# Kernel tuning notes

Hardware: AMD Instinct MI355X
Metric: run time of the kernel (lower is better)

The kernel has to match this reference:

```python
import jax, jax.numpy as jnp
import numpy as np

# dims matching init_kwargs
L, D, NH = 4, 1024, 16          # num_blocks, embed_dim, num_heads
HD = D // NH                     # head dim
CUR, MEM, BS, IN = 512, 512, 8, 512
FF = 4 * D
GRU_BIAS = 2.0

def sinusoidal_pe(full_seq, dim):
    # SinusoidalPE: freqs = arange(0, dim, 2); inv = 10000**(-freqs/dim); seq descending
    freqs = jnp.arange(0, dim, 2.0)
    inv = 10000.0 ** (-freqs / dim)
    seq = jnp.arange(full_seq - 1, -1, -1.0)
    ang = seq[:, None] * inv[None, :]                       # (full, dim/2)
    return jnp.concatenate([jnp.sin(ang), jnp.cos(ang)], axis=-1)  # (full, dim)

def layer_norm(x, g, b, eps=1e-5):
    m = x.mean(-1, keepdims=True)
    v = ((x - m) ** 2).mean(-1, keepdims=True)
    return (x - m) * jax.lax.rsqrt(v + eps) * g + b

def rel_shift(x):
    # Transformer-XL relative shift. x: (q, k, b, h)
    q, k, b, h = x.shape
    zp = jnp.zeros((q, 1, b, h), x.dtype)
    return jnp.concatenate([zp, x], axis=1).reshape(k + 1, q, b, h)[1:].reshape(q, k, b, h)

def gru_gate(x, y, W):
    # W: (6, D, D) = Wr, Ur, Wz, Uz, Wg, Ug (no bias except learned-ish gru_bias on z)
    Wr, Ur, Wz, Uz, Wg, Ug = W[0], W[1], W[2], W[3], W[4], W[5]
    r = jax.nn.sigmoid(y @ Wr.T + x @ Ur.T)
    z = jax.nn.sigmoid(y @ Wz.T + x @ Uz.T - GRU_BIAS)
    hh = jnp.tanh(y @ Wg.T + (r * x) @ Ug.T)
    return (1.0 - z) * x + z * hh

def rel_attn(q, k, v, pos, U, V, mask, W):
    # q: (cur, bs, D); k, v: (full, bs, D); pos: (full, D); W: (5, D, D) = Wq,Wk,Wv,Wr,Wo
    cur, bs, _ = q.shape
    full = k.shape[0]
    qh = (q @ W[0].T).reshape(cur, bs, NH, HD)
    kh = (k @ W[1].T).reshape(full, bs, NH, HD)
    vh = (v @ W[2].T).reshape(full, bs, NH, HD)
    rh = (pos @ W[3].T).reshape(full, NH, HD)
    AC = jnp.einsum('ibhd,jbhd->ijbh', qh + U, kh)          # content stream with U bias
    BD = rel_shift(jnp.einsum('ibhd,jhd->ijbh', qh + V, rh))  # position stream with V bias
    score = (AC + BD) * (1.0 / np.sqrt(HD))
    score = jnp.where(mask[:, :, None, None], jnp.asarray(-1e30, score.dtype), score)
    attn = jax.nn.softmax(score, axis=1)
    out = jnp.einsum('ijbh,jbhd->ibhd', attn, vh).reshape(cur, bs, D)
    return out @ W[4].T

def gelu(x):
    return jax.nn.gelu(x, approximate=False)  # torch nn.GELU default is exact

def _forward(h, memory, W_emb, b_emb, U, V, ln1, ln2, Wattn, g1, g2, fc_W1, fc_b1, fc_W2, fc_b2):
    h = jnp.transpose(h, (1, 0, 2))            # (cur, bs, in)
    mem = jax.lax.stop_gradient(memory)        # memory holds detached hidden states
    cur = h.shape[0]
    prev = mem.shape[1]
    full = cur + prev
    x = gelu(h @ W_emb.T + b_emb)              # linear embedding + GELU activation
    pos = sinusoidal_pe(full, D)               # (full, D); pos_emb.unsqueeze(1) broadcast over bs
    mask = jnp.triu(jnp.ones((cur, full), bool), 1 + prev)
    out = x
    for i in range(L):
        key = jnp.concatenate([mem[i], out], axis=0)   # (full, bs, D)
        nq = layer_norm(out, ln1[i, 0], ln1[i, 1])
        nk = layer_norm(key, ln1[i, 0], ln1[i, 1])
        Y = rel_attn(nq, nk, nk, pos, U, V, mask, Wattn[i])
        Y = gelu(Y)                                     # dropout is identity (eval / p=0)
        o1 = gru_gate(out, Y, g1[i])
        E = layer_norm(o1, ln2[i, 0], ln2[i, 1])
        E = gelu(gelu(E @ fc_W1[i].T + fc_b1[i]) @ fc_W2[i].T + fc_b2[i])
        out = gru_gate(o1, E, g2[i])
    return jnp.transpose(out, (1, 0, 2))       # (bs, cur, D)

def setup_inputs() -> dict:
    key = jax.random.key(0)
    ks = jax.random.split(key, 12)
    s = 0.02
    eye2 = jnp.stack([jnp.ones(D, jnp.float32), jnp.zeros(D, jnp.float32)])  # (gamma, beta)
    return {
        'h': jax.random.normal(ks[0], (BS, CUR, IN), jnp.float32),
        'memory': jax.random.normal(ks[1], (L, MEM, BS, D), jnp.float32),
        'W_emb': jax.random.normal(ks[2], (D, IN), jnp.float32) * s,
        'b_emb': jnp.zeros((D,), jnp.float32),
        'U': jax.random.normal(ks[3], (NH, HD), jnp.float32) * s,
        'V': jax.random.normal(ks[4], (NH, HD), jnp.float32) * s,
        'ln1': jnp.tile(eye2[None], (L, 1, 1)),
        'ln2': jnp.tile(eye2[None], (L, 1, 1)),
        'Wattn': jax.random.normal(ks[5], (L, 5, D, D), jnp.float32) * s,  # q,k,v,r,o per block
        'g1': jax.random.normal(ks[6], (L, 6, D, D), jnp.float32) * s,
        'g2': jax.random.normal(ks[7], (L, 6, D, D), jnp.float32) * s,
        'fc_W1': jax.random.normal(ks[8], (L, FF, D), jnp.float32) * s,
        'fc_b1': jnp.zeros((L, FF), jnp.float32),
        'fc_W2': jax.random.normal(ks[9], (L, D, FF), jnp.float32) * s,
        'fc_b2': jnp.zeros((L, D), jnp.float32),
    }

def reference(h, memory, W_emb, b_emb, U, V, ln1, ln2, Wattn, g1, g2, fc_W1, fc_b1, fc_W2, fc_b2):
    return _forward(h, memory, W_emb, b_emb, U, V, ln1, ln2, Wattn, g1, g2, fc_W1, fc_b1, fc_W2, fc_b2)
```

## Files before the change

### kernel.cpp

```cpp
#include <hip/hip_runtime.h>
#include <hip/hip_bf16.h>


typedef __attribute__((ext_vector_type(8))) __bf16 bfrag;
typedef __attribute__((ext_vector_type(4))) float f4;
typedef __attribute__((ext_vector_type(4))) unsigned short u16x4;
typedef __attribute__((ext_vector_type(8))) unsigned short u16x8;

__device__ __forceinline__ unsigned short f2bf(float f){
  union { float f; unsigned u; } v; v.f = f;
  unsigned r = v.u + 0x7fffu + ((v.u >> 16) & 1u);
  return (unsigned short)(r >> 16);
}
__device__ __forceinline__ float bf2f(unsigned short u){
  union { unsigned u; float f; } v; v.u = (unsigned)u << 16; return v.f;
}
__device__ __forceinline__ float geluf(float x){
  return 0.5f * x * (1.0f + erff(x * 0.7071067811865476f));
}
__device__ __forceinline__ float sigm(float x){ return 1.0f/(1.0f + __expf(-x)); }

__device__ __forceinline__ void gl_lds(const void* g, void* l){
  __builtin_amdgcn_global_load_lds(
    reinterpret_cast<const __attribute__((address_space(1))) unsigned int*>(
        reinterpret_cast<unsigned long>(g)),
    reinterpret_cast<__attribute__((address_space(3))) unsigned int*>(
        reinterpret_cast<unsigned long>(l)),
    16, 0, 0);
}

struct GP {
  const unsigned short* A;
  const unsigned short* A2;
  const unsigned short* B;
  const unsigned short* B2;
  unsigned short* O1;
  unsigned short* O2;
  unsigned short* O3;
  unsigned short* O4;
  unsigned short* O5;
  float* OF;
  const float* bias1;
  const float* bias2;
  const float* X;
  const float* Z;
  int K, Ksplit, lda, ldb, ldo;
  int sBz;
};

template<int BM, int BN, int EPI>
__global__ __launch_bounds__(256) void gemm_k(GP p){
  __shared__ unsigned short As[2][2][BM*32];
  __shared__ unsigned short Bs[2][2][BN*32];
  const int tid  = threadIdx.x;
  const int lane = tid & 63;
  const int wid  = tid >> 6;
  const int lr   = lane & 15;
  const int lg   = lane >> 4;
  constexpr int FM = BM/32, FN = BN/32;

  int bx = blockIdx.x, by = blockIdx.y;
  {
    const int gx = gridDim.x;
    const int nwg = gx * gridDim.y;
    if ((nwg & 7) == 0){
      const int bid = by*gx + bx;
      const int vid = (bid & 7)*(nwg >> 3) + (bid >> 3);
      bx = vid % gx;
      by = vid / gx;
    }
  }
  const int m0 = by * BM;
  const int n0 = bx * BN;
  const int z  = blockIdx.z;

  const unsigned short* Abase = p.A;
  const unsigned short* Bbase = p.B;
  if constexpr (EPI==13){
    if (z==2){ if (by >= 32) return; Abase = p.A + 4194304; }
    if (z==3){ if (by >= 8)  return; Abase = p.A2; }
    const int zsel = (z==0)?1:((z==1)?2:((z==2)?0:3));
    Bbase = p.B + (long)zsel*1048576;
  }

  const int ksp = p.Ksplit ? p.Ksplit : p.K;
  const unsigned short* AbL = Abase + (long)m0*p.lda;
  const unsigned short* AbH = p.A2 && EPI!=13 ? (p.A2 + (long)m0*p.lda - ksp) : AbL;
  const unsigned short* BbL = Bbase + (long)z*p.sBz + (long)n0*p.ldb;
  const unsigned short* BbH = p.B2 ? (p.B2 + (long)z*p.sBz + (long)n0*p.ldb - ksp) : BbL;

  const int srow = tid >> 2;
  const int skk  = (tid & 3) * 8;

  f4 acc[FM][FN];
  f4 zero4 = {0.0f, 0.0f, 0.0f, 0.0f};
  #pragma unroll
  for (int m=0;m<FM;m++)
    #pragma unroll
    for (int n=0;n<FN;n++) acc[m][n] = zero4;

  auto stage = [&](int buf, int sub, int k0){
    const unsigned short* A_ = (k0 < ksp) ? AbL : AbH;
    #pragma unroll
    for (int q=0;q<BM/64;q++)
      gl_lds(A_ + (long)(q*64 + srow)*p.lda + k0 + skk, (char*)As[buf][sub] + q*4096 + wid*1024);
    const unsigned short* B_ = (k0 < ksp) ? BbL : BbH;
    #pragma unroll
    for (int q=0;q<BN/64;q++)
      gl_lds(B_ + (long)(q*64 + srow)*p.ldb + k0 + skk, (char*)Bs[buf][sub] + q*4096 + wid*1024);
  };

  const int nk2 = p.K >> 6;
  stage(0,0,0); stage(0,1,32);
  __syncthreads();

  int cur = 0;
  for (int t = 0; t < nk2; ++t){
    if (t+1 < nk2){
      stage(cur^1, 0, (t+1)*64);
      stage(cur^1, 1, (t+1)*64 + 32);
    }
    #pragma unroll
    for (int sub=0; sub<2; ++sub){
      bfrag af[FM], bfr[FN];
      #pragma unroll
      for (int m=0;m<FM;m++)
        af[m] = *(const bfrag*)&As[cur][sub][((wid>>1)*(BM/2) + m*16 + lr)*32 + lg*8];
      #pragma unroll
      for (int n=0;n<FN;n++)
        bfr[n] = *(const bfrag*)&Bs[cur][sub][((wid&1)*(BN/2) + n*16 + lr)*32 + lg*8];
      #pragma unroll
      for (int m=0;m<FM;m++)
        #pragma unroll
        for (int n=0;n<FN;n++)
          acc[m][n] = __builtin_amdgcn_mfma_f32_16x16x32_bf16(af[m], bfr[n], acc[m][n], 0, 0, 0);
    }
    __syncthreads();
    cur ^= 1;
  }

  const int wr0 = m0 + (wid>>1)*(BM/2);
  const int wc0 = n0 + (wid&1)*(BN/2);
  #pragma unroll
  for (int m=0;m<FM;m++)
    #pragma unroll
    for (int n=0;n<FN;n++)
      #pragma unroll
      for (int r=0;r<4;r++){
        const int gr = wr0 + m*16 + lg*4 + r;
        const int gc = wc0 + n*16 + lr;
        const float a = acc[m][n][r];
        const long base = (long)gr*p.ldo + gc;
        if constexpr (EPI==6){
          const float t = a + (p.bias1 ? p.bias1[gc] : 0.0f);
          p.O1[base] = f2bf(geluf(t));
        }
        else if constexpr (EPI==7){
          const float t = geluf(a + p.bias1[gc]);
          p.OF[base] = t; p.O1[base] = f2bf(t);
        }
        else if constexpr (EPI==11){
          const long ix = (long)gr*1024 + gc;
          if (z==0) p.O1[ix] = f2bf(sigm(a) * p.X[ix]);
          else      p.OF[ix] = sigm(a - 2.0f);
        }
        else if constexpr (EPI==12){
          const long ix = (long)gr*1024 + gc;
          const float zz = p.Z[ix];
          const float oo = (1.0f - zz)*p.X[ix] + zz*tanhf(a);
          p.OF[ix] = oo; p.O1[ix] = f2bf(oo);
        }
        else if constexpr (EPI==13){
          const long ix = (long)gr*1024 + gc;
          if (z==0){ p.O1[ix] = f2bf(a); }
          else if (z==1){
            const int b_ = gr & 7, js = gr >> 3, h_ = gc >> 6, d_ = gc & 63;
            p.O2[(long)(b_*16 + h_)*65536 + (long)d_*1024 + js] = f2bf(a);
          }
          else if (z==2){ p.O3[ix] = f2bf((a + p.bias1[gc])*0.125f);
                          p.O4[ix] = f2bf((a + p.bias2[gc])*0.125f); }
          else { p.O5[ix] = f2bf(a); }
        }
      }
}

__global__ __launch_bounds__(256,4) void attn_k(const unsigned short* __restrict__ qU,
                                                const unsigned short* __restrict__ qV,
                                                const unsigned short* __restrict__ kh,
                                                const unsigned short* __restrict__ rh,
                                                const unsigned short* __restrict__ vhT,
                                                unsigned short* __restrict__ ctx){
  __shared__ char Sm[20480];
  __shared__ float redm[4][16];
  __shared__ float reds[4][16];
  __shared__ float invd[16];
  const int tid = threadIdx.x;
  const int w   = tid >> 6;
  const int lane= tid & 63;
  const int lr  = lane & 15;
  const int lg  = lane >> 4;
  const int id = blockIdx.x;
  const int b  = id & 7;
  const int i0 = ((id >> 3) & 31) * 16;
  const int h  = id >> 8;
  const int gmax = i0 >> 4;
  const long hoff = (long)h * 64;
  const f4 z4 = {0.f,0.f,0.f,0.f};

  bfrag bqv[2];
  #pragma unroll
  for (int kk=0;kk<2;kk++)
    bqv[kk] = *(const bfrag*)(qV + ((long)(i0 + lr)*8 + b)*1024 + hoff + kk*32 + lg*8);
  bfrag aq[2];
  #pragma unroll
  for (int kk=0;kk<2;kk++)
    aq[kk] = *(const bfrag*)(qU + ((long)(i0 + lr)*8 + b)*1024 + hoff + kk*32 + lg*8);

  f4 s[16];
  #pragma unroll
  for (int n=0;n<16;n++) s[n] = (f4){-1e30f,-1e30f,-1e30f,-1e30f};

  #pragma unroll
  for (int half=0; half<2; ++half){
    const int c0    = half*512;
    const int rbase = half ? (1008 - i0) : (496 - i0);
    const int ntil  = half ? (gmax + 1) : 33;
    const int radd  = half ? -497 : 15;
    for (int mt = w; mt < ntil; mt += 4){
      const int r0 = rbase + mt*16;
      f4 acc = z4;
      #pragma unroll
      for (int kk=0;kk<2;kk++){
        bfrag ar = *(const bfrag*)(rh + (long)(r0 + lr)*1024 + hoff + kk*32 + lg*8);
        acc = __builtin_amdgcn_mfma_f32_16x16x32_bf16(ar, bqv[kk], acc, 0,0,0);
      }
      #pragma unroll
      for (int q=0;q<4;q++){
        const int rr = mt*16 + lg*4 + q;
        *(unsigned short*)(Sm + rr*38 + lr*2) = f2bf(acc[q]);
      }
    }
    __syncthreads();
    #pragma unroll
    for (int n=0;n<8;n++){
      const int g = 2*w + ((n>>1)<<3) + (n&1);
      if (half==1 && g > gmax) continue;
      const int cb = c0 + w*32 + (n>>1)*128 + (n&1)*16;
      f4 a = z4;
      #pragma unroll
      for (int kk=0;kk<2;kk++){
        bfrag bk = *(const bfrag*)(kh + ((long)(cb + lr)*8 + b)*1024 + hoff + kk*32 + lg*8);
        a = __builtin_amdgcn_mfma_f32_16x16x32_bf16(aq[kk], bk, a, 0,0,0);
      }
      #pragma unroll
      for (int q=0;q<4;q++){
        const int di = lg*4 + q;
        const int jc = cb + lr;
        if (jc > i0 + di + 512) a[q] = -1e30f;
        else {
          const int rr = jc - di + radd;
          a[q] += bf2f(*(const unsigned short*)(Sm + rr*38 + di*2));
        }
      }
      s[half*8 + n] = a;
    }
    __syncthreads();
  }

  float mx[4], sum[4];
  #pragma unroll
  for (int q=0;q<4;q++){
    float m = s[0][q];
    #pragma unroll
    for (int n=1;n<16;n++) m = fmaxf(m, s[n][q]);
    m = fmaxf(m, __shfl_xor(m, 1));
    m = fmaxf(m, __shfl_xor(m, 2));
    m = fmaxf(m, __shfl_xor(m, 4));
    m = fmaxf(m, __shfl_xor(m, 8));
    if (lr == 0) redm[w][lg*4+q] = m;
  }
  __syncthreads();
  #pragma unroll
  for (int q=0;q<4;q++){
    const int row = lg*4+q;
    mx[q] = fmaxf(fmaxf(redm[0][row], redm[1][row]), fmaxf(redm[2][row], redm[3][row]));
    sum[q] = 0.0f;
  }
  #pragma unroll
  for (int n=0;n<16;n++)
    #pragma unroll
    for (int q=0;q<4;q++){
      const float e = __expf(s[n][q] - mx[q]);
      s[n][q] = e;
      sum[q] += e;
    }
  #pragma unroll
  for (int q=0;q<4;q++){
    float v = sum[q];
    v += __shfl_xor(v, 1);
    v += __shfl_xor(v, 2);
    v += __shfl_xor(v, 4);
    v += __shfl_xor(v, 8);
    if (lr == 0) reds[w][lg*4+q] = v;
  }
  __syncthreads();
  if (tid < 16)
    invd[tid] = 1.0f / (reds[0][tid] + reds[1][tid] + reds[2][tid] + reds[3][tid]);

  f4 oac[4];
  #pragma unroll
  for (int nd=0;nd<4;nd++) oac[nd] = z4;
  const unsigned short* vb_base = vhT + (long)(b*16 + h)*65536;
  char* Pch = Sm + w*1024;
  #pragma unroll
  for (int t=0;t<8;t++){
    const int hh_ = t>>2, tt = t&3;
    if (hh_==1 && (2*w + 8*tt) > gmax) continue;
    const int jb = hh_*512 + w*32 + tt*128;
    #pragma unroll
    for (int nn=0;nn<2;nn++){
      const f4 e = s[hh_*8 + tt*2 + nn];
      #pragma unroll
      for (int q=0;q<4;q++){
        const int row = lg*4 + q;
        const int col = nn*16 + lr;
        *(unsigned short*)(Pch + row*64 + ((col*2) ^ (((row>>2)&3)<<4))) = f2bf(e[q]);
      }
    }
    bfrag pa = *(const bfrag*)(Pch + lr*64 + ((lg*16) ^ (((lr>>2)&3)<<4)));
    #pragma unroll
    for (int nd=0;nd<4;nd++){
      bfrag bv = *(const bfrag*)(vb_base + (long)(nd*16 + lr)*1024 + jb + lg*8);
      oac[nd] = __builtin_amdgcn_mfma_f32_16x16x32_bf16(pa, bv, oac[nd], 0,0,0);
    }
  }
  float* po = (float*)(Sm + 4096 + w*4096);
  #pragma unroll
  for (int nd=0;nd<4;nd++)
    #pragma unroll
    for (int q=0;q<4;q++)
      po[(lg*4+q)*64 + nd*16 + lr] = oac[nd][q];
  __syncthreads();
  {
    const int row = tid >> 4;
    const int d0  = (tid & 15) * 4;
    f4 v = *(const f4*)(Sm + 4096 + (row*64 + d0)*4);
    #pragma unroll
    for (int ww=1;ww<4;ww++){
      const f4 u = *(const f4*)(Sm + 4096 + ww*4096 + (row*64 + d0)*4);
      v.x += u.x; v.y += u.y; v.z += u.z; v.w += u.w;
    }
    const float iv = invd[row];
    u16x4 o;
    o.x = f2bf(v.x*iv); o.y = f2bf(v.y*iv); o.z = f2bf(v.z*iv); o.w = f2bf(v.w*iv);
    *(u16x4*)(ctx + ((long)(i0 + row)*8 + b)*1024 + hoff + d0) = o;
  }
}

__global__ __launch_bounds__(256) void ln_k(const float* __restrict__ srcA,
                                            const float* __restrict__ srcB, int splitRow,
                                            const float* __restrict__ g, const float* __restrict__ b,
                                            unsigned short* __restrict__ dst){
  const int row = blockIdx.x;
  const float* src = (srcB != nullptr && row >= splitRow)
                       ? (srcB + (long)(row - splitRow)*1024)
                       : (srcA + (long)row*1024);
  const int t = threadIdx.x;
  float4 v = ((const float4*)src)[t];
  float s1 = v.x+v.y+v.z+v.w;
  float s2 = v.x*v.x+v.y*v.y+v.z*v.z+v.w*v.w;
  #pragma unroll
  for (int o=32;o;o>>=1){ s1 += __shfl_xor(s1,o); s2 += __shfl_xor(s2,o); }
  __shared__ float r1[4], r2[4];
  const int w = t>>6;
  if ((t&63)==0){ r1[w]=s1; r2[w]=s2; }
  __syncthreads();
  s1 = r1[0]+r1[1]+r1[2]+r1[3];
  s2 = r2[0]+r2[1]+r2[2]+r2[3];
  const float mean = s1*(1.0f/1024.0f);
  const float var  = s2*(1.0f/1024.0f) - mean*mean;
  const float rs   = rsqrtf(var + 1e-5f);
  float4 gg = ((const float4*)g)[t];
  float4 bb = ((const float4*)b)[t];
  u16x4 o;
  o.x = f2bf((v.x-mean)*rs*gg.x + bb.x);
  o.y = f2bf((v.y-mean)*rs*gg.y + bb.y);
  o.z = f2bf((v.z-mean)*rs*gg.z + bb.z);
  o.w = f2bf((v.w-mean)*rs*gg.w + bb.w);
  *(u16x4*)(dst + (long)row*1024 + t*4) = o;
}

__global__ __launch_bounds__(256) void conv_k(const float* __restrict__ s,
                                              unsigned short* __restrict__ d, long n){
  long i = ((long)blockIdx.x*256 + threadIdx.x)*4;
  if (i >= n) return;
  float4 v = *(const float4*)(s + i);
  u16x4 o; o.x=f2bf(v.x); o.y=f2bf(v.y); o.z=f2bf(v.z); o.w=f2bf(v.w);
  *(u16x4*)(d + i) = o;
}

__global__ __launch_bounds__(256) void conv5_k(const float* __restrict__ wat,
                                               const float* __restrict__ g1,
                                               const float* __restrict__ g2,
                                               const float* __restrict__ f1,
                                               const float* __restrict__ f2,
                                               unsigned short* __restrict__ dst){
  const long i = ((long)blockIdx.x*256 + threadIdx.x)*4;
  const float* s; long off;
  if      (i <  5242880){ s = wat; off = 0; }
  else if (i < 11534336){ s = g1;  off = 5242880; }
  else if (i < 17825792){ s = g2;  off = 11534336; }
  else if (i < 22020096){ s = f1;  off = 17825792; }
  else                  { s = f2;  off = 22020096; }
  float4 v = *(const float4*)(s + (i - off));
  u16x4 o; o.x=f2bf(v.x); o.y=f2bf(v.y); o.z=f2bf(v.z); o.w=f2bf(v.w);
  *(u16x4*)(dst + i) = o;
}

__global__ __launch_bounds__(128) void ht_k(const float* __restrict__ h,
                                            unsigned short* __restrict__ d){
  const int row = blockIdx.x;
  const int i = row>>3, b = row&7;
  const float* src = h + ((long)b*512 + i)*512;
  const int t = threadIdx.x;
  float4 v = ((const float4*)src)[t];
  u16x4 o; o.x=f2bf(v.x); o.y=f2bf(v.y); o.z=f2bf(v.z); o.w=f2bf(v.w);
  *(u16x4*)(d + (long)row*512 + t*4) = o;
}

__global__ __launch_bounds__(256) void pos_k(unsigned short* __restrict__ d){
  const int r = blockIdx.x, t = threadIdx.x;
  const float seq = (float)(1023 - r);
  u16x4 o;
  #pragma unroll
  for (int q=0;q<4;q++){
    const int c = t*4 + q;
    const int f = (c < 512) ? c : (c - 512);
    const float inv = expf((float)f * -0.017988946039016f);
    const float ang = seq * inv;
    const float val = (c < 512) ? sinf(ang) : cosf(ang);
    o[q] = f2bf(val);
  }
  *(u16x4*)(d + (long)r*1024 + t*4) = o;
}

__global__ __launch_bounds__(256) void outT_k(const float* __restrict__ o,
                                              float* __restrict__ d){
  const int row = blockIdx.x;
  const int b = row>>9, i = row&511;
  const float4 v = ((const float4*)(o + ((long)i*8 + b)*1024))[threadIdx.x];
  ((float4*)(d + (long)row*1024))[threadIdx.x] = v;
}

extern "C" void kernel_launch(void* const* d_in, const int* in_sizes, int n_in,
                              void* d_out, int out_size, void* d_ws, size_t ws_size,
                              hipStream_t stream){
  (void)in_sizes; (void)n_in; (void)out_size; (void)ws_size;
  const float* h     = (const float*)d_in[0];
  const float* memin = (const float*)d_in[1];
  const float* Wemb  = (const float*)d_in[2];
  const float* bemb  = (const float*)d_in[3];
  const float* Ub    = (const float*)d_in[4];
  const float* Vb    = (const float*)d_in[5];
  const float* ln1   = (const float*)d_in[6];
  const float* ln2   = (const float*)d_in[7];
  const float* Wattn = (const float*)d_in[8];
  const float* g1w   = (const float*)d_in[9];
  const float* g2w   = (const float*)d_in[10];
  const float* fw1   = (const float*)d_in[11];
  const float* fb1   = (const float*)d_in[12];
  const float* fw2   = (const float*)d_in[13];
  const float* fb2   = (const float*)d_in[14];

  char* Wp = (char*)d_ws;
  size_t off = 0;
  auto take = [&](size_t bytes)->size_t{ size_t r = off; off += (bytes + 255) & ~(size_t)255; return r; };
  float*          outf = (float*)         (Wp + take(16777216));
  unsigned short* xbf  = (unsigned short*)(Wp + take( 8388608));
  float*          o1f  = (float*)         (Wp + take(16777216));
  unsigned short* o1b  = (unsigned short*)(Wp + take( 8388608));
  float*          zbf  = (float*)         (Wp + take(16777216));
  unsigned short* rxb  = (unsigned short*)(Wp + take( 8388608));
  unsigned short* yb   = (unsigned short*)(Wp + take( 8388608));
  unsigned short* Eb   = (unsigned short*)(Wp + take( 8388608));
  unsigned short* wb0  = (unsigned short*)(Wp + take(52428800));
  unsigned short* hTb  = (unsigned short*)(Wp + take( 4194304));
  unsigned short* webb = (unsigned short*)(Wp + take( 1048576));
  unsigned short* posb = (unsigned short*)(Wp + take( 2097152));
  unsigned short* nkb  = (unsigned short*)(Wp + take(16777216));
  unsigned short* qUb  = (unsigned short*)(Wp + take( 8388608));
  unsigned short* qVb  = (unsigned short*)(Wp + take( 8388608));
  unsigned short* khb  = (unsigned short*)(Wp + take(16777216));
  unsigned short* vhTb = (unsigned short*)(Wp + take(16777216));
  unsigned short* F1b  = khb;
  unsigned short* rhb  = (unsigned short*)(Wp + take( 2097152));
  unsigned short* ctxb = (unsigned short*)(Wp + take( 8388608));

  const int M1 = 1048576;

  conv_k<<<512, 256, 0, stream>>>(Wemb, webb, 524288);
  ht_k<<<4096, 128, 0, stream>>>(h, hTb);
  pos_k<<<1024, 256, 0, stream>>>(posb);

  {
    GP p{}; p.A=hTb; p.B=webb; p.OF=outf; p.O1=xbf; p.bias1=bemb;
    p.K=512; p.lda=512; p.ldb=512; p.ldo=1024;
    gemm_k<128,64,7><<<dim3(16,32,1),256,0,stream>>>(p);
  }

  auto gru_fn = [&](const unsigned short* xb, const float* xf, const unsigned short* yb_,
                    const unsigned short* w6, float* of, unsigned short* ob){
    { GP p{}; p.A=yb_; p.A2=xb; p.B=w6; p.B2=w6+M1; p.sBz=2*M1;
      p.O1=rxb; p.OF=zbf; p.X=xf;
      p.K=2048; p.Ksplit=1024; p.lda=1024; p.ldb=1024; p.ldo=1024;
      gemm_k<128,64,11><<<dim3(16,32,2),256,0,stream>>>(p); }
    { GP p{}; p.A=yb_; p.A2=rxb; p.B=w6+4*M1; p.B2=w6+5*M1;
      p.X=xf; p.Z=zbf; p.OF=of; p.O1=ob;
      p.K=2048; p.Ksplit=1024; p.lda=1024; p.ldb=1024; p.ldo=1024;
      gemm_k<128,64,12><<<dim3(16,32,1),256,0,stream>>>(p); }
  };

  for (int l = 0; l < 4; ++l){
    conv5_k<<<25600,256,0,stream>>>(Wattn + (long)l*5242880,
                                    g1w   + (long)l*6291456,
                                    g2w   + (long)l*6291456,
                                    fw1   + (long)l*4194304,
                                    fw2   + (long)l*4194304, wb0);

    ln_k<<<8192,256,0,stream>>>(memin + (long)l*4194304, outf, 4096,
                                ln1 + l*2048, ln1 + l*2048 + 1024, nkb);

    {
      GP p{}; p.A=nkb; p.A2=posb; p.B=wb0;
      p.O1=khb; p.O2=vhTb; p.O3=qUb; p.O4=qVb; p.O5=rhb;
      p.bias1=Ub; p.bias2=Vb;
      p.K=1024; p.lda=1024; p.ldb=1024; p.ldo=1024;
      gemm_k<128,64,13><<<dim3(16,64,4),256,0,stream>>>(p); }

    attn_k<<<4096,256,0,stream>>>(qUb, qVb, khb, rhb, vhTb, ctxb);

    {
      GP p{}; p.A=ctxb; p.B=wb0+4*M1; p.O1=yb;
      p.K=1024; p.lda=1024; p.ldb=1024; p.ldo=1024;
      gemm_k<128,64,6><<<dim3(16,32,1),256,0,stream>>>(p); }

    gru_fn(xbf, outf, yb, wb0 + 5*M1, o1f, o1b);

    ln_k<<<4096,256,0,stream>>>(o1f, nullptr, 1<<30,
                                ln2 + l*2048, ln2 + l*2048 + 1024, Eb);

    { GP p{}; p.A=Eb;  p.B=wb0+17*M1; p.O1=F1b; p.bias1=fb1 + l*4096;
      p.K=1024; p.lda=1024; p.ldb=1024; p.ldo=4096;
      gemm_k<128,64,6><<<dim3(64,32,1),256,0,stream>>>(p); }
    { GP p{}; p.A=F1b; p.B=wb0+21*M1; p.O1=yb; p.bias1=fb2 + l*1024;
      p.K=4096; p.lda=4096; p.ldb=4096; p.ldo=1024;
      gemm_k<128,64,6><<<dim3(16,32,1),256,0,stream>>>(p); }

    gru_fn(o1b, o1f, yb, wb0 + 11*M1, outf, xbf);
  }

  outT_k<<<4096,256,0,stream>>>(outf, (float*)d_out);
}
```

Measured before the change: 2.687 ms.

## Software-pipeline K and V loads in attention kernel with MFMA priority hints

Restructures the attention kernel's QK and PV loops into explicitly software-pipelined stages. K fragments are loaded two tiles ahead using rotating register buffers, and V fragments one tile ahead, with the first V load issued before the softmax reductions. MFMA sections are wrapped in s_setprio, and the column tile assignment is remapped (interleaved w+4n). Occupancy hint drops from 4 to 3 blocks per CU to make room for the extra live registers. This risks lower occupancy and must keep the causal tile skipping and V column mapping consistent.

```diff
diff --git a/kernel.cpp b/kernel.cpp
--- a/kernel.cpp
+++ b/kernel.cpp
@@ -184,7 +184,7 @@
       }
 }
 
-__global__ __launch_bounds__(256,4) void attn_k(const unsigned short* __restrict__ qU,
+__global__ __launch_bounds__(256,3) void attn_k(const unsigned short* __restrict__ qU,
                                                 const unsigned short* __restrict__ qV,
                                                 const unsigned short* __restrict__ kh,
                                                 const unsigned short* __restrict__ rh,
@@ -216,9 +216,38 @@
   for (int kk=0;kk<2;kk++)
     aq[kk] = *(const bfrag*)(qU + ((long)(i0 + lr)*8 + b)*1024 + hoff + kk*32 + lg*8);
 
+  const int nv1 = (gmax >= w) ? (((gmax - w) >> 2) + 1) : 0;
+
   f4 s[16];
-  #pragma unroll
-  for (int n=0;n<16;n++) s[n] = (f4){-1e30f,-1e30f,-1e30f,-1e30f};
+
+#define LDK(DST, n_) { \
+    const int cbx = c0 + (w + 4*(n_))*16; \
+    DST[0] = *(const bfrag*)(kh + ((long)(cbx + lr)*8 + b)*1024 + hoff + lg*8); \
+    DST[1] = *(const bfrag*)(kh + ((long)(cbx + lr)*8 + b)*1024 + hoff + 32 + lg*8); }
+
+#define AC_CMP(n_, CUR) { \
+    const int cbx = c0 + (w + 4*(n_))*16; \
+    f4 a = z4; \
+    __builtin_amdgcn_s_setprio(1); \
+    a = __builtin_amdgcn_mfma_f32_16x16x32_bf16(aq[0], CUR[0], a, 0,0,0); \
+    a = __builtin_amdgcn_mfma_f32_16x16x32_bf16(aq[1], CUR[1], a, 0,0,0); \
+    __builtin_amdgcn_s_setprio(0); \
+    _Pragma("unroll") \
+    for (int q=0;q<4;q++){ \
+      const int di = lg*4 + q; \
+      const int jc = cbx + lr; \
+      if (jc > i0 + di + 512) a[q] = -1e30f; \
+      else { \
+        const int rr = jc - di + radd; \
+        a[q] += bf2f(*(const unsigned short*)(Sm + rr*38 + di*2)); \
+      } \
+    } \
+    s[half*8 + n_] = a; }
+
+#define AC_STEP(n_, CUR, NXT) \
+    if ((n_)+2 < nv) LDK(NXT, (n_)+2); \
+    if ((n_) < nv) AC_CMP(n_, CUR) \
+    else s[half*8 + n_] = (f4){-1e30f,-1e30f,-1e30f,-1e30f};
 
   #pragma unroll
   for (int half=0; half<2; ++half){
@@ -241,31 +270,39 @@
       }
     }
     __syncthreads();
-    #pragma unroll
-    for (int n=0;n<8;n++){
-      const int g = 2*w + ((n>>1)<<3) + (n&1);
-      if (half==1 && g > gmax) continue;
-      const int cb = c0 + w*32 + (n>>1)*128 + (n&1)*16;
-      f4 a = z4;
-      #pragma unroll
-      for (int kk=0;kk<2;kk++){
-        bfrag bk = *(const bfrag*)(kh + ((long)(cb + lr)*8 + b)*1024 + hoff + kk*32 + lg*8);
-        a = __builtin_amdgcn_mfma_f32_16x16x32_bf16(aq[kk], bk, a, 0,0,0);
-      }
-      #pragma unroll
-      for (int q=0;q<4;q++){
-        const int di = lg*4 + q;
-        const int jc = cb + lr;
-        if (jc > i0 + di + 512) a[q] = -1e30f;
-        else {
-          const int rr = jc - di + radd;
-          a[q] += bf2f(*(const unsigned short*)(Sm + rr*38 + di*2));
-        }
-      }
-      s[half*8 + n] = a;
+    const int nv = (half==0) ? 8 : nv1;
+    {
+      bfrag bkA[2], bkB[2], bkC[2];
+      if (0 < nv) LDK(bkA, 0);
+      if (1 < nv) LDK(bkB, 1);
+      AC_STEP(0, bkA, bkC)
+      AC_STEP(1, bkB, bkA)
+      AC_STEP(2, bkC, bkB)
+      AC_STEP(3, bkA, bkC)
+      AC_STEP(4, bkB, bkA)
+      AC_STEP(5, bkC, bkB)
+      AC_STEP(6, bkA, bkC)
+      AC_STEP(7, bkB, bkA)
     }
     __syncthreads();
   }
+
+  const unsigned short* vb_base = vhT + (long)(b*16 + h)*65536;
+
+#define LDV(DST, t_) { \
+    const int c0v = ((t_) >> 2) * 512; \
+    const int tau = (t_) & 3; \
+    const int jA = c0v + (w + 8*tau)*16; \
+    const int jB = c0v + (w + 8*tau + 4)*16; \
+    const int jcol = (lg < 2) ? (jA + lg*8) : (jB + (lg-2)*8); \
+    _Pragma("unroll") \
+    for (int nd=0; nd<4; nd++) \
+      DST[nd] = *(const bfrag*)(vb_base + (long)(nd*16 + lr)*1024 + jcol); }
+
+#define CHV(t_) ((t_) < 4 || (2*((t_)-4) < nv1))
+
+  bfrag vbA[4], vbB[4];
+  LDV(vbA, 0);
 
   float mx[4], sum[4];
   #pragma unroll
@@ -310,30 +347,39 @@
   f4 oac[4];
   #pragma unroll
   for (int nd=0;nd<4;nd++) oac[nd] = z4;
-  const unsigned short* vb_base = vhT + (long)(b*16 + h)*65536;
   char* Pch = Sm + w*1024;
-  #pragma unroll
-  for (int t=0;t<8;t++){
-    const int hh_ = t>>2, tt = t&3;
-    if (hh_==1 && (2*w + 8*tt) > gmax) continue;
-    const int jb = hh_*512 + w*32 + tt*128;
-    #pragma unroll
-    for (int nn=0;nn<2;nn++){
-      const f4 e = s[hh_*8 + tt*2 + nn];
-      #pragma unroll
-      for (int q=0;q<4;q++){
-        const int row = lg*4 + q;
-        const int col = nn*16 + lr;
-        *(unsigned short*)(Pch + row*64 + ((col*2) ^ (((row>>2)&3)<<4))) = f2bf(e[q]);
-      }
-    }
-    bfrag pa = *(const bfrag*)(Pch + lr*64 + ((lg*16) ^ (((lr>>2)&3)<<4)));
-    #pragma unroll
-    for (int nd=0;nd<4;nd++){
-      bfrag bv = *(const bfrag*)(vb_base + (long)(nd*16 + lr)*1024 + jb + lg*8);
-      oac[nd] = __builtin_amdgcn_mfma_f32_16x16x32_bf16(pa, bv, oac[nd], 0,0,0);
-    }
-  }
+
+#define PV_STEP(t_, CUR, NXT) \
+    if ((t_)+1 < 8 && CHV((t_)+1)) LDV(NXT, (t_)+1); \
+    if (CHV(t_)){ \
+      const int s0i = (((t_)<4)?0:8) + ((t_)&3)*2; \
+      _Pragma("unroll") \
+      for (int nn=0;nn<2;nn++){ \
+        const f4 e = s[s0i + nn]; \
+        _Pragma("unroll") \
+        for (int q=0;q<4;q++){ \
+          const int row = lg*4 + q; \
+          const int col = nn*16 + lr; \
+          *(unsigned short*)(Pch + row*64 + ((col*2) ^ (((row>>2)&3)<<4))) = f2bf(e[q]); \
+        } \
+      } \
+      bfrag pa = *(const bfrag*)(Pch + lr*64 + ((lg*16) ^ (((lr>>2)&3)<<4))); \
+      __builtin_amdgcn_s_setprio(1); \
+      _Pragma("unroll") \
+      for (int nd=0;nd<4;nd++) \
+        oac[nd] = __builtin_amdgcn_mfma_f32_16x16x32_bf16(pa, CUR[nd], oac[nd], 0,0,0); \
+      __builtin_amdgcn_s_setprio(0); \
+    }
+
+  PV_STEP(0, vbA, vbB)
+  PV_STEP(1, vbB, vbA)
+  PV_STEP(2, vbA, vbB)
+  PV_STEP(3, vbB, vbA)
+  PV_STEP(4, vbA, vbB)
+  PV_STEP(5, vbB, vbA)
+  PV_STEP(6, vbA, vbB)
+  PV_STEP(7, vbB, vbA)
+
   float* po = (float*)(Sm + 4096 + w*4096);
   #pragma unroll
   for (int nd=0;nd<4;nd++)
@@ -355,6 +401,12 @@
     o.x = f2bf(v.x*iv); o.y = f2bf(v.y*iv); o.z = f2bf(v.z*iv); o.w = f2bf(v.w*iv);
     *(u16x4*)(ctx + ((long)(i0 + row)*8 + b)*1024 + hoff + d0) = o;
   }
+#undef LDK
+#undef AC_CMP
+#undef AC_STEP
+#undef LDV
+#undef CHV
+#undef PV_STEP
 }
 
 __global__ __launch_bounds__(256) void ln_k(const float* __restrict__ srcA,
```

After: 2.693 ms. Within noise of the previous version (+0.2%).
